# Kernel tuning notes

Hardware: AMD Instinct MI355X
Metric: run time of the kernel (lower is better)

Reference implementation:

```python
import jax, jax.numpy as jnp
import numpy as np

B, N, E, H = 8, 2048, 1024, 16
D = E // H

def setup_inputs() -> dict:
    key = jax.random.key(0)
    kx, kw1, kb1, kw2, kb2 = jax.random.split(key, 5)
    scale = 0.02
    return {
        "x": jax.random.normal(kx, (B, N, E), dtype=jnp.float32),
        "Wqkv": jax.random.normal(kw1, (3 * E, E), dtype=jnp.float32) * scale,
        "bqkv": jax.random.normal(kb1, (3 * E,), dtype=jnp.float32) * scale,
        "Wo": jax.random.normal(kw2, (E, E), dtype=jnp.float32) * scale,
        "bo": jax.random.normal(kb2, (E,), dtype=jnp.float32) * scale,
    }

def reference(x, Wqkv, bqkv, Wo, bo):
    b, n, e = x.shape
    h, d = H, D
    # qkv projection: torch Linear is x @ W.T + b
    qkv = x @ Wqkv.T + bqkv                                   # [B,N,3E]
    qkv = qkv.reshape(b, n, 3, h, d).transpose(2, 0, 3, 1, 4)  # [3,B,H,N,D]
    q, k, v = qkv[0], qkv[1], qkv[2]                           # each [B,H,N,D]
    # NOTE: replicates the original's einsum labeling exactly: with q,k of
    # shape [B,H,N,D], 'nqhd,nkhd->nhqk' contracts over D and yields [B,N,H,H]
    # (softmax over the head axis), matching the torch source bit-for-bit.
    energy = jnp.einsum('nqhd,nkhd->nhqk', q, k)               # [B,N,H,H]
    attention = jax.nn.softmax(energy / jnp.sqrt(jnp.float32(e)), axis=-1)
    out = jnp.einsum('nhql,nlhd->nqhd', attention, v)          # [B,H,N,D]
    out = out.reshape(b, n, e)                                 # same raw-buffer reshape as torch
    return out @ Wo.T + bo
```

## Files before the change

### kernel.cpp

```cpp
#include <hip/hip_runtime.h>
#include <hip/hip_bf16.h>
#include <stdint.h>


typedef __attribute__((ext_vector_type(8))) short short8;
typedef __attribute__((ext_vector_type(8))) unsigned short ushort8;
typedef __attribute__((ext_vector_type(16))) float floatx16;

__device__ __forceinline__ unsigned short f2bf(float f) {
  union { float f; uint32_t u; } x; x.f = f;
  uint32_t u = x.u;
  return (unsigned short)((u + 0x7fffu + ((u >> 16) & 1u)) >> 16);
}
__device__ __forceinline__ float bf2f(unsigned short s) {
  union { uint32_t u; float f; } x; x.u = ((uint32_t)s) << 16; return x.f;
}

__global__ __launch_bounds__(256) void cvt_kernel(const float* __restrict__ in,
                                                  unsigned short* __restrict__ out, int n8) {
  int i = blockIdx.x * 256 + threadIdx.x;
  if (i >= n8) return;
  long base = (long)i * 8;
  const float4* p = (const float4*)(in + base);
  float4 a = p[0], b = p[1];
  ushort8 r;
  r[0] = f2bf(a.x); r[1] = f2bf(a.y); r[2] = f2bf(a.z); r[3] = f2bf(a.w);
  r[4] = f2bf(b.x); r[5] = f2bf(b.y); r[6] = f2bf(b.z); r[7] = f2bf(b.w);
  *(ushort8*)(out + base) = r;
}

__device__ __forceinline__ void gl2lds16(const void* g, void* l) {
  __builtin_amdgcn_global_load_lds(
      (const uint32_t __attribute__((address_space(1)))*)g,
      (uint32_t __attribute__((address_space(3)))*)(uint32_t)(uintptr_t)l,
      16, 0, 0);
}

template <bool OUT_BF16>
__device__ __forceinline__ void gemm_core(const unsigned short* __restrict__ A,
                                          const unsigned short* __restrict__ Bm,
                                          const float* __restrict__ bias,
                                          void* __restrict__ Cout, int N, int K) {
  __shared__ __align__(16) unsigned short lA[128 * 64];
  __shared__ __align__(16) unsigned short lB[128 * 64];
  const int tid = threadIdx.x;
  const int lane = tid & 63;
  const int wave = tid >> 6;
  const long row0 = (long)blockIdx.y * 128;
  const long col0 = (long)blockIdx.x * 128;
  const int wr = (wave & 1) * 64;
  const int wc = (wave >> 1) * 64;
  const int l32 = lane & 31;
  const int lhi = lane >> 5;
  const int l7 = lane & 7;

  floatx16 acc[2][2] = {};

  const int rstage = tid >> 3;
  const int cstage = (tid & 7) ^ (rstage & 7);
  const unsigned short* gA0 = A + (row0 + rstage) * (long)K + cstage * 8;
  const unsigned short* gB0 = Bm + (col0 + rstage) * (long)K + cstage * 8;
  char* ldsA0 = (char*)lA + tid * 16;
  char* ldsB0 = (char*)lB + tid * 16;
  const long rowstep = (long)32 * K;

  int aRow[2], bRow[2], sOff[4];
#pragma unroll
  for (int i = 0; i < 2; i++) aRow[i] = (wr + i * 32 + l32) * 128;
#pragma unroll
  for (int j = 0; j < 2; j++) bRow[j] = (wc + j * 32 + l32) * 128;
#pragma unroll
  for (int s = 0; s < 4; s++) sOff[s] = ((2 * s + lhi) ^ l7) * 16;

  for (int k0 = 0; k0 < K; k0 += 64) {
    __syncthreads();
#pragma unroll
    for (int p = 0; p < 4; p++) {
      gl2lds16(gA0 + p * rowstep + k0, ldsA0 + p * 4096);
      gl2lds16(gB0 + p * rowstep + k0, ldsB0 + p * 4096);
    }
    __syncthreads();

#pragma unroll
    for (int s = 0; s < 4; s++) {
      short8 a0 = *(const short8*)((char*)lA + aRow[0] + sOff[s]);
      short8 a1 = *(const short8*)((char*)lA + aRow[1] + sOff[s]);
      short8 b0 = *(const short8*)((char*)lB + bRow[0] + sOff[s]);
      short8 b1 = *(const short8*)((char*)lB + bRow[1] + sOff[s]);
      acc[0][0] = __builtin_amdgcn_mfma_f32_32x32x16_bf16(a0, b0, acc[0][0], 0, 0, 0);
      acc[0][1] = __builtin_amdgcn_mfma_f32_32x32x16_bf16(a0, b1, acc[0][1], 0, 0, 0);
      acc[1][0] = __builtin_amdgcn_mfma_f32_32x32x16_bf16(a1, b0, acc[1][0], 0, 0, 0);
      acc[1][1] = __builtin_amdgcn_mfma_f32_32x32x16_bf16(a1, b1, acc[1][1], 0, 0, 0);
    }
  }

  float bv[2];
#pragma unroll
  for (int j = 0; j < 2; j++) bv[j] = bias[col0 + wc + j * 32 + l32];

#pragma unroll
  for (int i = 0; i < 2; i++) {
#pragma unroll
    for (int j = 0; j < 2; j++) {
      const long col = col0 + wc + j * 32 + l32;
      const long rbase = row0 + wr + i * 32 + 4 * lhi;
#pragma unroll
      for (int reg = 0; reg < 16; reg++) {
        const long row = rbase + (reg & 3) + 8 * (reg >> 2);
        float v = acc[i][j][reg] + bv[j];
        if (OUT_BF16)
          ((unsigned short*)Cout)[row * N + col] = f2bf(v);
        else
          ((float*)Cout)[row * N + col] = v;
      }
    }
  }
}

__global__ __launch_bounds__(256) void gemm_qkv(const unsigned short* __restrict__ A,
                                                const unsigned short* __restrict__ Bm,
                                                const float* __restrict__ bias,
                                                unsigned short* __restrict__ Cout,
                                                int N, int K) {
  gemm_core<true>(A, Bm, bias, Cout, N, K);
}

__global__ __launch_bounds__(256) void gemm_out(const unsigned short* __restrict__ A,
                                                const unsigned short* __restrict__ Bm,
                                                const float* __restrict__ bias,
                                                float* __restrict__ Cout,
                                                int N, int K) {
  gemm_core<false>(A, Bm, bias, Cout, N, K);
}

__global__ __launch_bounds__(256) void attn_kernel(const unsigned short* __restrict__ qkv,
                                                   unsigned short* __restrict__ out2) {
  const int t = blockIdx.x * 256 + threadIdx.x;
  const int head = t & 15;
  const int token = t >> 4;
  const int b = token >> 11;
  const int s = token & 2047;
  const unsigned short* base = qkv + (long)token * 3072;

  float qf[64];
  {
    const uint4* qp = (const uint4*)(base + head * 64);
#pragma unroll
    for (int w = 0; w < 8; w++) {
      uint4 u = qp[w];
      uint32_t arr[4] = {u.x, u.y, u.z, u.w};
#pragma unroll
      for (int c = 0; c < 4; c++) {
        qf[w * 8 + c * 2 + 0] = bf2f((unsigned short)(arr[c] & 0xffffu));
        qf[w * 8 + c * 2 + 1] = bf2f((unsigned short)(arr[c] >> 16));
      }
    }
  }

  float e[16];
  const unsigned short* kbase = base + 1024;
  for (int j = 0; j < 16; j++) {
    const uint4* kp = (const uint4*)(kbase + j * 64);
    float acc = 0.f;
#pragma unroll
    for (int w = 0; w < 8; w++) {
      uint4 u = kp[w];
      uint32_t arr[4] = {u.x, u.y, u.z, u.w};
#pragma unroll
      for (int c = 0; c < 4; c++) {
        acc += qf[w * 8 + c * 2 + 0] * bf2f((unsigned short)(arr[c] & 0xffffu));
        acc += qf[w * 8 + c * 2 + 1] * bf2f((unsigned short)(arr[c] >> 16));
      }
    }
    e[j] = acc * 0.03125f;
  }

  float mx = e[0];
#pragma unroll
  for (int j = 1; j < 16; j++) mx = fmaxf(mx, e[j]);
  float p[16];
  float sum = 0.f;
#pragma unroll
  for (int j = 0; j < 16; j++) { p[j] = __expf(e[j] - mx); sum += p[j]; }
  const float inv = 1.f / sum;

  float o[64];
#pragma unroll
  for (int d = 0; d < 64; d++) o[d] = 0.f;
  const unsigned short* vbase = base + 2048;
  for (int j = 0; j < 16; j++) {
    const float wgt = p[j] * inv;
    const uint4* vp = (const uint4*)(vbase + j * 64);
#pragma unroll
    for (int w = 0; w < 8; w++) {
      uint4 u = vp[w];
      uint32_t arr[4] = {u.x, u.y, u.z, u.w};
#pragma unroll
      for (int c = 0; c < 4; c++) {
        o[w * 8 + c * 2 + 0] += wgt * bf2f((unsigned short)(arr[c] & 0xffffu));
        o[w * 8 + c * 2 + 1] += wgt * bf2f((unsigned short)(arr[c] >> 16));
      }
    }
  }

  const long row = (long)b * 2048 + head * 128 + (s >> 4);
  unsigned short* op = out2 + row * 1024 + (long)(s & 15) * 64;
#pragma unroll
  for (int w = 0; w < 8; w++) {
    ushort8 r;
#pragma unroll
    for (int c = 0; c < 8; c++) r[c] = f2bf(o[w * 8 + c]);
    *(ushort8*)(op + w * 8) = r;
  }
}

extern "C" void kernel_launch(void* const* d_in, const int* in_sizes, int n_in,
                              void* d_out, int out_size, void* d_ws, size_t ws_size,
                              hipStream_t stream) {
  const float* x    = (const float*)d_in[0];
  const float* Wqkv = (const float*)d_in[1];
  const float* bqkv = (const float*)d_in[2];
  const float* Wo   = (const float*)d_in[3];
  const float* bo   = (const float*)d_in[4];
  float* out = (float*)d_out;

  char* ws = (char*)d_ws;
  unsigned short* x_bf    = (unsigned short*)(ws);
  unsigned short* wqkv_bf = (unsigned short*)(ws + 33554432);
  unsigned short* wo_bf   = (unsigned short*)(ws + 39845888);
  unsigned short* qkv_bf  = (unsigned short*)(ws + 41943040);
  unsigned short* out2_bf = (unsigned short*)(ws + 142606336);

  cvt_kernel<<<8192, 256, 0, stream>>>(x, x_bf, 16777216 / 8);
  cvt_kernel<<<1536, 256, 0, stream>>>(Wqkv, wqkv_bf, 3145728 / 8);
  cvt_kernel<<<512, 256, 0, stream>>>(Wo, wo_bf, 1048576 / 8);

  dim3 g1(3072 / 128, 16384 / 128);
  gemm_qkv<<<g1, 256, 0, stream>>>(x_bf, wqkv_bf, bqkv, qkv_bf, 3072, 1024);

  attn_kernel<<<1024, 256, 0, stream>>>(qkv_bf, out2_bf);

  dim3 g2(1024 / 128, 16384 / 128);
  gemm_out<<<g2, 256, 0, stream>>>(out2_bf, wo_bf, bo, out, 1024, 1024);
}
```

Baseline: 357.8 us.

## Split attention head across four lanes and merge conversion kernels

```diff
diff --git a/kernel.cpp b/kernel.cpp
--- a/kernel.cpp
+++ b/kernel.cpp
@@ -15,18 +15,36 @@
 __device__ __forceinline__ float bf2f(unsigned short s) {
   union { uint32_t u; float f; } x; x.u = ((uint32_t)s) << 16; return x.f;
 }
-
-__global__ __launch_bounds__(256) void cvt_kernel(const float* __restrict__ in,
-                                                  unsigned short* __restrict__ out, int n8) {
+__device__ __forceinline__ void unpack8(uint4 u, float* f) {
+  f[0] = bf2f((unsigned short)(u.x & 0xffffu)); f[1] = bf2f((unsigned short)(u.x >> 16));
+  f[2] = bf2f((unsigned short)(u.y & 0xffffu)); f[3] = bf2f((unsigned short)(u.y >> 16));
+  f[4] = bf2f((unsigned short)(u.z & 0xffffu)); f[5] = bf2f((unsigned short)(u.z >> 16));
+  f[6] = bf2f((unsigned short)(u.w & 0xffffu)); f[7] = bf2f((unsigned short)(u.w >> 16));
+}
+
+__global__ __launch_bounds__(256) void cvt_all(const float* __restrict__ x,
+                                               const float* __restrict__ w1,
+                                               const float* __restrict__ w2,
+                                               unsigned short* __restrict__ xb,
+                                               unsigned short* __restrict__ w1b,
+                                               unsigned short* __restrict__ w2b) {
   int i = blockIdx.x * 256 + threadIdx.x;
-  if (i >= n8) return;
+  const float* src;
+  unsigned short* dst;
+  if (i < 2097152) {
+    src = x; dst = xb;
+  } else if (i < 2097152 + 393216) {
+    i -= 2097152; src = w1; dst = w1b;
+  } else {
+    i -= 2490368; src = w2; dst = w2b;
+  }
   long base = (long)i * 8;
-  const float4* p = (const float4*)(in + base);
+  const float4* p = (const float4*)(src + base);
   float4 a = p[0], b = p[1];
   ushort8 r;
   r[0] = f2bf(a.x); r[1] = f2bf(a.y); r[2] = f2bf(a.z); r[3] = f2bf(a.w);
   r[4] = f2bf(b.x); r[5] = f2bf(b.y); r[6] = f2bf(b.z); r[7] = f2bf(b.w);
-  *(ushort8*)(out + base) = r;
+  *(ushort8*)(dst + base) = r;
 }
 
 __device__ __forceinline__ void gl2lds16(const void* g, void* l) {
@@ -136,77 +154,68 @@
 __global__ __launch_bounds__(256) void attn_kernel(const unsigned short* __restrict__ qkv,
                                                    unsigned short* __restrict__ out2) {
   const int t = blockIdx.x * 256 + threadIdx.x;
-  const int head = t & 15;
-  const int token = t >> 4;
+  const int sub = t & 3;
+  const int pair = t >> 2;
+  const int head = pair & 15;
+  const int token = pair >> 4;
   const int b = token >> 11;
   const int s = token & 2047;
   const unsigned short* base = qkv + (long)token * 3072;
 
-  float qf[64];
+  float qf[16];
   {
-    const uint4* qp = (const uint4*)(base + head * 64);
-#pragma unroll
-    for (int w = 0; w < 8; w++) {
-      uint4 u = qp[w];
-      uint32_t arr[4] = {u.x, u.y, u.z, u.w};
-#pragma unroll
-      for (int c = 0; c < 4; c++) {
-        qf[w * 8 + c * 2 + 0] = bf2f((unsigned short)(arr[c] & 0xffffu));
-        qf[w * 8 + c * 2 + 1] = bf2f((unsigned short)(arr[c] >> 16));
-      }
-    }
+    const uint4* qp = (const uint4*)(base + head * 64 + sub * 16);
+    unpack8(qp[0], qf);
+    unpack8(qp[1], qf + 8);
   }
 
   float e[16];
-  const unsigned short* kbase = base + 1024;
+  const unsigned short* kbase = base + 1024 + sub * 16;
   for (int j = 0; j < 16; j++) {
     const uint4* kp = (const uint4*)(kbase + j * 64);
-    float acc = 0.f;
-#pragma unroll
-    for (int w = 0; w < 8; w++) {
-      uint4 u = kp[w];
-      uint32_t arr[4] = {u.x, u.y, u.z, u.w};
-#pragma unroll
-      for (int c = 0; c < 4; c++) {
-        acc += qf[w * 8 + c * 2 + 0] * bf2f((unsigned short)(arr[c] & 0xffffu));
-        acc += qf[w * 8 + c * 2 + 1] * bf2f((unsigned short)(arr[c] >> 16));
-      }
-    }
-    e[j] = acc * 0.03125f;
+    float kf[16];
+    unpack8(kp[0], kf);
+    unpack8(kp[1], kf + 8);
+    float a0 = 0.f, a1 = 0.f, a2 = 0.f, a3 = 0.f;
+#pragma unroll
+    for (int c = 0; c < 4; c++) {
+      a0 += qf[c] * kf[c];
+      a1 += qf[c + 4] * kf[c + 4];
+      a2 += qf[c + 8] * kf[c + 8];
+      a3 += qf[c + 12] * kf[c + 12];
+    }
+    float ej = (a0 + a1) + (a2 + a3);
+    ej += __shfl_xor(ej, 1);
+    ej += __shfl_xor(ej, 2);
+    e[j] = ej * 0.03125f;
   }
 
   float mx = e[0];
 #pragma unroll
   for (int j = 1; j < 16; j++) mx = fmaxf(mx, e[j]);
-  float p[16];
   float sum = 0.f;
 #pragma unroll
-  for (int j = 0; j < 16; j++) { p[j] = __expf(e[j] - mx); sum += p[j]; }
+  for (int j = 0; j < 16; j++) { e[j] = __expf(e[j] - mx); sum += e[j]; }
   const float inv = 1.f / sum;
 
-  float o[64];
-#pragma unroll
-  for (int d = 0; d < 64; d++) o[d] = 0.f;
-  const unsigned short* vbase = base + 2048;
+  float o[16];
+#pragma unroll
+  for (int d = 0; d < 16; d++) o[d] = 0.f;
+  const unsigned short* vbase = base + 2048 + sub * 16;
   for (int j = 0; j < 16; j++) {
-    const float wgt = p[j] * inv;
+    const float wgt = e[j] * inv;
     const uint4* vp = (const uint4*)(vbase + j * 64);
-#pragma unroll
-    for (int w = 0; w < 8; w++) {
-      uint4 u = vp[w];
-      uint32_t arr[4] = {u.x, u.y, u.z, u.w};
-#pragma unroll
-      for (int c = 0; c < 4; c++) {
-        o[w * 8 + c * 2 + 0] += wgt * bf2f((unsigned short)(arr[c] & 0xffffu));
-        o[w * 8 + c * 2 + 1] += wgt * bf2f((unsigned short)(arr[c] >> 16));
-      }
-    }
+    float vf[16];
+    unpack8(vp[0], vf);
+    unpack8(vp[1], vf + 8);
+#pragma unroll
+    for (int d = 0; d < 16; d++) o[d] += wgt * vf[d];
   }
 
   const long row = (long)b * 2048 + head * 128 + (s >> 4);
-  unsigned short* op = out2 + row * 1024 + (long)(s & 15) * 64;
-#pragma unroll
-  for (int w = 0; w < 8; w++) {
+  unsigned short* op = out2 + row * 1024 + (long)(s & 15) * 64 + sub * 16;
+#pragma unroll
+  for (int w = 0; w < 2; w++) {
     ushort8 r;
 #pragma unroll
     for (int c = 0; c < 8; c++) r[c] = f2bf(o[w * 8 + c]);
@@ -231,14 +240,12 @@
   unsigned short* qkv_bf  = (unsigned short*)(ws + 41943040);
   unsigned short* out2_bf = (unsigned short*)(ws + 142606336);
 
-  cvt_kernel<<<8192, 256, 0, stream>>>(x, x_bf, 16777216 / 8);
-  cvt_kernel<<<1536, 256, 0, stream>>>(Wqkv, wqkv_bf, 3145728 / 8);
-  cvt_kernel<<<512, 256, 0, stream>>>(Wo, wo_bf, 1048576 / 8);
+  cvt_all<<<10240, 256, 0, stream>>>(x, Wqkv, Wo, x_bf, wqkv_bf, wo_bf);
 
   dim3 g1(3072 / 128, 16384 / 128);
   gemm_qkv<<<g1, 256, 0, stream>>>(x_bf, wqkv_bf, bqkv, qkv_bf, 3072, 1024);
 
-  attn_kernel<<<1024, 256, 0, stream>>>(qkv_bf, out2_bf);
+  attn_kernel<<<4096, 256, 0, stream>>>(qkv_bf, out2_bf);
 
   dim3 g2(1024 / 128, 16384 / 128);
   gemm_out<<<g2, 256, 0, stream>>>(out2_bf, wo_bf, bo, out, 1024, 1024);
```

After: 340.9 us. -4.7%, faster.
